# Performance work log

Measured on AMD Instinct MI355X. Metric: run time of the kernel, lower is better.

Reference implementation:

```python
import jax, jax.numpy as jnp
import numpy as np

FILLER = 10.1  # filler_value from __init__
B, C, L, KEEP = 128, 16, 16384, 12288


def setup_inputs() -> dict:
    key = jax.random.key(0)
    k1, k2, k3, k4 = jax.random.split(key, 4)
    x1 = jax.random.normal(k1, (B, C, 4096), dtype=jnp.float32)
    x2 = jax.random.normal(k2, (B, C, 4096), dtype=jnp.float32)
    x3 = jax.random.normal(k3, (B, C, L), dtype=jnp.float32)
    # Scatter exactly (L - KEEP) filler entries at random positions in every row,
    # so per-row compaction yields a uniform length KEEP (required by np.stack
    # in the original module).
    u = jax.random.uniform(k4, (B, C, L))
    ranks = jnp.argsort(jnp.argsort(u, axis=-1), axis=-1)  # random permutation ranks
    fill_mask = ranks < (L - KEEP)
    x3 = jnp.where(fill_mask, jnp.float32(FILLER), x3)
    return {"x1": x1, "x2": x2, "x3": x3, "keep_len": KEEP}


def reference(x1, x2, x3, keep_len):
    # Per-row stream compaction: drop entries equal to FILLER, keep original
    # order of survivors, output fixed length keep_len.
    is_filler = x3 == jnp.float32(FILLER)          # [B, C, L] bool
    # Stable argsort moves non-filler (False=0) to the front, order-preserving.
    order = jnp.argsort(is_filler, axis=-1, stable=True)  # [B, C, L]
    compacted = jnp.take_along_axis(x3, order, axis=-1)    # [B, C, L]
    return compacted[..., :keep_len]                        # [B, C, keep_len]
```

## Files before the change

### kernel.cpp

```cpp
#include <hip/hip_runtime.h>


#define FILLER_VAL 10.1f
constexpr int L_LEN    = 16384;
constexpr int KEEP_LEN = 12288;
constexpr int BLOCK    = 256;
constexpr int NW       = BLOCK / 64;
constexpr int CHUNK    = BLOCK * 4;
constexpr int NC       = L_LEN / CHUNK;

__global__ __launch_bounds__(BLOCK, 6) void compact_rows_kernel(
    const float* __restrict__ x3, float* __restrict__ out)
{
    const int row = blockIdx.x;
    const float* __restrict__ in = x3 + (size_t)row * L_LEN;
    float* __restrict__ o = out + (size_t)row * KEEP_LEN;

    const int tid  = threadIdx.x;
    const int lane = tid & 63;
    const int wid  = tid >> 6;
    const unsigned long long lt = (1ULL << lane) - 1ULL;

    __shared__ unsigned short stage[KEEP_LEN];
    __shared__ int wtot[NC][NW];

    int pk[NC];
    #pragma unroll
    for (int c = 0; c < NC; ++c) {
        const float4 v = *reinterpret_cast<const float4*>(in + c * CHUNK + tid * 4);
        const unsigned long long m0 = __ballot(v.x != FILLER_VAL);
        const unsigned long long m1 = __ballot(v.y != FILLER_VAL);
        const unsigned long long m2 = __ballot(v.z != FILLER_VAL);
        const unsigned long long m3 = __ballot(v.w != FILLER_VAL);
        const int before = __popcll(m0 & lt) + __popcll(m1 & lt)
                         + __popcll(m2 & lt) + __popcll(m3 & lt);
        const int bits = (int)((m0 >> lane) & 1ULL)
                       | ((int)((m1 >> lane) & 1ULL) << 1)
                       | ((int)((m2 >> lane) & 1ULL) << 2)
                       | ((int)((m3 >> lane) & 1ULL) << 3);
        pk[c] = bits | (before << 4);
        if (lane == 0)
            wtot[c][wid] = __popcll(m0) + __popcll(m1)
                         + __popcll(m2) + __popcll(m3);
    }
    __syncthreads();

    int run = 0;
    #pragma unroll
    for (int c = 0; c < NC; ++c) {
        int wb = run;
        #pragma unroll
        for (int w = 0; w < NW; ++w) {
            const int t = wtot[c][w];
            if (w < wid) wb += t;
            run += t;
        }
        const int bits   = pk[c] & 15;
        const int before = pk[c] >> 4;
        const int p0 = wb + before;
        const int p1 = p0 + (bits & 1);
        const int p2 = p1 + ((bits >> 1) & 1);
        const int p3 = p2 + ((bits >> 2) & 1);
        const int idx = c * CHUNK + tid * 4;
        if ((bits & 1) && p0 < KEEP_LEN) stage[p0] = (unsigned short)(idx);
        if ((bits & 2) && p1 < KEEP_LEN) stage[p1] = (unsigned short)(idx + 1);
        if ((bits & 4) && p2 < KEEP_LEN) stage[p2] = (unsigned short)(idx + 2);
        if ((bits & 8) && p3 < KEEP_LEN) stage[p3] = (unsigned short)(idx + 3);
    }
    __syncthreads();

    #pragma unroll
    for (int it = 0; it < KEEP_LEN / (BLOCK * 8); ++it) {
        const int o0 = it * (BLOCK * 8) + tid * 4;
        const int o1 = o0 + BLOCK * 4;
        const ushort4 i0 = *reinterpret_cast<const ushort4*>(&stage[o0]);
        const ushort4 i1 = *reinterpret_cast<const ushort4*>(&stage[o1]);
        float4 a, b;
        a.x = in[i0.x]; a.y = in[i0.y]; a.z = in[i0.z]; a.w = in[i0.w];
        b.x = in[i1.x]; b.y = in[i1.y]; b.z = in[i1.z]; b.w = in[i1.w];
        *reinterpret_cast<float4*>(&o[o0]) = a;
        *reinterpret_cast<float4*>(&o[o1]) = b;
    }
}

extern "C" void kernel_launch(void* const* d_in, const int* in_sizes, int n_in,
                              void* d_out, int out_size, void* d_ws, size_t ws_size,
                              hipStream_t stream)
{
    const float* x3 = (const float*)d_in[2];
    float* out = (float*)d_out;

    const int rows = in_sizes[2] / L_LEN;

    compact_rows_kernel<<<rows, BLOCK, 0, stream>>>(x3, out);
}
```

Measured before the change: 272.0 us.

## Stage compacted values in LDS from registers instead of gathering indices from global

Each row is now loaded once into registers as float4s. The surviving values are scattered into a float LDS buffer, then written out with coalesced float4 stores. This replaces the old scheme of staging 16-bit indices and doing a second, scalar, uncoalesced gather from global memory. Each block now handles two rows and the launch-bounds occupancy hint drops from 6 to 3. The cost is more register pressure (64 values held live) and a larger 48KB LDS footprint per block, which limits blocks per CU.

```diff
diff --git a/kernel.cpp b/kernel.cpp
--- a/kernel.cpp
+++ b/kernel.cpp
@@ -8,78 +8,80 @@
 constexpr int NW       = BLOCK / 64;
 constexpr int CHUNK    = BLOCK * 4;
 constexpr int NC       = L_LEN / CHUNK;
+constexpr int RPB      = 2;
 
-__global__ __launch_bounds__(BLOCK, 6) void compact_rows_kernel(
-    const float* __restrict__ x3, float* __restrict__ out)
+__global__ __launch_bounds__(BLOCK, 3) void compact_rows_kernel(
+    const float* __restrict__ x3, float* __restrict__ out, int rows)
 {
-    const int row = blockIdx.x;
-    const float* __restrict__ in = x3 + (size_t)row * L_LEN;
-    float* __restrict__ o = out + (size_t)row * KEEP_LEN;
-
     const int tid  = threadIdx.x;
     const int lane = tid & 63;
     const int wid  = tid >> 6;
     const unsigned long long lt = (1ULL << lane) - 1ULL;
 
-    __shared__ unsigned short stage[KEEP_LEN];
+    __shared__ float stage[KEEP_LEN];
     __shared__ int wtot[NC][NW];
 
-    int pk[NC];
     #pragma unroll
-    for (int c = 0; c < NC; ++c) {
-        const float4 v = *reinterpret_cast<const float4*>(in + c * CHUNK + tid * 4);
-        const unsigned long long m0 = __ballot(v.x != FILLER_VAL);
-        const unsigned long long m1 = __ballot(v.y != FILLER_VAL);
-        const unsigned long long m2 = __ballot(v.z != FILLER_VAL);
-        const unsigned long long m3 = __ballot(v.w != FILLER_VAL);
-        const int before = __popcll(m0 & lt) + __popcll(m1 & lt)
-                         + __popcll(m2 & lt) + __popcll(m3 & lt);
-        const int bits = (int)((m0 >> lane) & 1ULL)
-                       | ((int)((m1 >> lane) & 1ULL) << 1)
-                       | ((int)((m2 >> lane) & 1ULL) << 2)
-                       | ((int)((m3 >> lane) & 1ULL) << 3);
-        pk[c] = bits | (before << 4);
-        if (lane == 0)
-            wtot[c][wid] = __popcll(m0) + __popcll(m1)
-                         + __popcll(m2) + __popcll(m3);
-    }
-    __syncthreads();
+    for (int r = 0; r < RPB; ++r) {
+        const int row = blockIdx.x * RPB + r;
+        if (row >= rows) break;
+        const float* __restrict__ in = x3 + (size_t)row * L_LEN;
+        float* __restrict__ o = out + (size_t)row * KEEP_LEN;
 
-    int run = 0;
-    #pragma unroll
-    for (int c = 0; c < NC; ++c) {
-        int wb = run;
+        float4 v[NC];
         #pragma unroll
-        for (int w = 0; w < NW; ++w) {
-            const int t = wtot[c][w];
-            if (w < wid) wb += t;
-            run += t;
+        for (int c = 0; c < NC; ++c)
+            v[c] = *reinterpret_cast<const float4*>(in + c * CHUNK + tid * 4);
+
+        int pk[NC];
+        #pragma unroll
+        for (int c = 0; c < NC; ++c) {
+            const unsigned long long m0 = __ballot(v[c].x != FILLER_VAL);
+            const unsigned long long m1 = __ballot(v[c].y != FILLER_VAL);
+            const unsigned long long m2 = __ballot(v[c].z != FILLER_VAL);
+            const unsigned long long m3 = __ballot(v[c].w != FILLER_VAL);
+            const int before = __popcll(m0 & lt) + __popcll(m1 & lt)
+                             + __popcll(m2 & lt) + __popcll(m3 & lt);
+            const int bits = (int)((m0 >> lane) & 1ULL)
+                           | ((int)((m1 >> lane) & 1ULL) << 1)
+                           | ((int)((m2 >> lane) & 1ULL) << 2)
+                           | ((int)((m3 >> lane) & 1ULL) << 3);
+            pk[c] = bits | (before << 4);
+            if (lane == 0)
+                wtot[c][wid] = __popcll(m0) + __popcll(m1)
+                             + __popcll(m2) + __popcll(m3);
         }
-        const int bits   = pk[c] & 15;
-        const int before = pk[c] >> 4;
-        const int p0 = wb + before;
-        const int p1 = p0 + (bits & 1);
-        const int p2 = p1 + ((bits >> 1) & 1);
-        const int p3 = p2 + ((bits >> 2) & 1);
-        const int idx = c * CHUNK + tid * 4;
-        if ((bits & 1) && p0 < KEEP_LEN) stage[p0] = (unsigned short)(idx);
-        if ((bits & 2) && p1 < KEEP_LEN) stage[p1] = (unsigned short)(idx + 1);
-        if ((bits & 4) && p2 < KEEP_LEN) stage[p2] = (unsigned short)(idx + 2);
-        if ((bits & 8) && p3 < KEEP_LEN) stage[p3] = (unsigned short)(idx + 3);
-    }
-    __syncthreads();
+        __syncthreads();
 
-    #pragma unroll
-    for (int it = 0; it < KEEP_LEN / (BLOCK * 8); ++it) {
-        const int o0 = it * (BLOCK * 8) + tid * 4;
-        const int o1 = o0 + BLOCK * 4;
-        const ushort4 i0 = *reinterpret_cast<const ushort4*>(&stage[o0]);
-        const ushort4 i1 = *reinterpret_cast<const ushort4*>(&stage[o1]);
-        float4 a, b;
-        a.x = in[i0.x]; a.y = in[i0.y]; a.z = in[i0.z]; a.w = in[i0.w];
-        b.x = in[i1.x]; b.y = in[i1.y]; b.z = in[i1.z]; b.w = in[i1.w];
-        *reinterpret_cast<float4*>(&o[o0]) = a;
-        *reinterpret_cast<float4*>(&o[o1]) = b;
+        int run = 0;
+        #pragma unroll
+        for (int c = 0; c < NC; ++c) {
+            int wb = run;
+            #pragma unroll
+            for (int w = 0; w < NW; ++w) {
+                const int t = wtot[c][w];
+                if (w < wid) wb += t;
+                run += t;
+            }
+            const int bits   = pk[c] & 15;
+            const int before = pk[c] >> 4;
+            const int p0 = wb + before;
+            const int p1 = p0 + (bits & 1);
+            const int p2 = p1 + ((bits >> 1) & 1);
+            const int p3 = p2 + ((bits >> 2) & 1);
+            if ((bits & 1) && p0 < KEEP_LEN) stage[p0] = v[c].x;
+            if ((bits & 2) && p1 < KEEP_LEN) stage[p1] = v[c].y;
+            if ((bits & 4) && p2 < KEEP_LEN) stage[p2] = v[c].z;
+            if ((bits & 8) && p3 < KEEP_LEN) stage[p3] = v[c].w;
+        }
+        __syncthreads();
+
+        #pragma unroll
+        for (int k = 0; k < KEEP_LEN / (BLOCK * 4); ++k) {
+            const int idx = (k * BLOCK + tid) * 4;
+            *reinterpret_cast<float4*>(&o[idx]) =
+                *reinterpret_cast<const float4*>(&stage[idx]);
+        }
     }
 }
 
@@ -91,6 +93,7 @@
     float* out = (float*)d_out;
 
     const int rows = in_sizes[2] / L_LEN;
+    const int grid = (rows + RPB - 1) / RPB;
 
-    compact_rows_kernel<<<rows, BLOCK, 0, stream>>>(x3, out);
+    compact_rows_kernel<<<grid, BLOCK, 0, stream>>>(x3, out, rows);
 }
```

After: 255.9 us. 1.06x faster.
